# Performance work log

Measured on AMD Instinct MI355X. Metric: run time of the kernel, lower is better.

Reference implementation:

```python
import jax, jax.numpy as jnp
import numpy as np

B, C, H, W = 8, 256, 96, 96
CQ = C // 8

def conv1x1(x, w, b):
    # x: (B,C,H,W), w: (O,C), b: (O,)
    return jnp.einsum('bchw,oc->bohw', x, w) + b[None, :, None, None]

def axial_attend(q, k, v):
    # q,k: (B,CQ,H,W); v: (B,C,H,W). Criss-cross attention with masked diagonal
    # on the column (H) branch and joint softmax over H+W logits.
    Hn = q.shape[2]
    e_h = jnp.einsum('bchw,bcgw->bhwg', q, k)            # (B,H,W,H), g = h'
    eye = jnp.eye(Hn, dtype=bool)
    e_h = jnp.where(eye[None, :, None, :], -jnp.inf, e_h)  # mask h'==h (self on column)
    e_w = jnp.einsum('bchw,bchv->bhwv', q, k)            # (B,H,W,W), v = w'
    attn = jax.nn.softmax(jnp.concatenate([e_h, e_w], axis=-1), axis=-1)
    a_h, a_w = attn[..., :Hn], attn[..., Hn:]
    out_h = jnp.einsum('bcgw,bhwg->bchw', v, a_h)
    out_w = jnp.einsum('bchv,bhwv->bchw', v, a_w)
    return out_h + out_w

def setup_inputs() -> dict:
    key = jax.random.key(0)
    ks = jax.random.split(key, 16)
    s = lambda k, shape, scale=1.0: (jax.random.normal(k, shape, dtype=jnp.float32) * scale)
    return {
        'x0': s(ks[0], (B, C, H, W)),
        'x1': s(ks[1], (B, C, H, W)),
        'wq0': s(ks[2], (CQ, C), 0.06), 'bq0': s(ks[3], (CQ,), 0.06),
        'wk0': s(ks[4], (CQ, C), 0.06), 'bk0': s(ks[5], (CQ,), 0.06),
        'wv0': s(ks[6], (C, C), 0.06),  'bv0': s(ks[7], (C,), 0.06),
        'wq1': s(ks[8], (CQ, C), 0.06), 'bq1': s(ks[9], (CQ,), 0.06),
        'wk1': s(ks[10], (CQ, C), 0.06), 'bk1': s(ks[11], (CQ,), 0.06),
        'wv1': s(ks[12], (C, C), 0.06),  'bv1': s(ks[13], (C,), 0.06),
        'gamma': s(ks[14], (1,)),
    }

def reference(x0, x1, wq0, bq0, wk0, bk0, wv0, bv0, wq1, bq1, wk1, bk1, wv1, bv1, gamma):
    q0 = conv1x1(x0, wq0, bq0); k0 = conv1x1(x0, wk0, bk0); v0 = conv1x1(x0, wv0, bv0)
    q1 = conv1x1(x1, wq1, bq1); k1 = conv1x1(x1, wk1, bk1); v1 = conv1x1(x1, wv1, bv1)
    g = gamma[0]
    # stream 0 output: queries from stream 1, keys/values from stream 0
    cat0 = g * axial_attend(q1, k0, v0) + x0
    # stream 1 output: queries from stream 0, keys/values from stream 1
    cat1 = g * axial_attend(q0, k1, v1) + x1
    return (cat0, cat1)
```

## Files before the change

kernel.cpp:

```cpp
#include <hip/hip_runtime.h>
#include <hip/hip_bf16.h>


#define Bn 8
#define Cn 256
#define NHW 9216
#define PT_BS ((size_t)NHW * 64)

typedef unsigned short u16;
typedef __attribute__((ext_vector_type(8))) _Float16 f16x8;
typedef __attribute__((ext_vector_type(4))) float f32x4;

__device__ __forceinline__ float h2f(u16 v) {
  _Float16 h;
  __builtin_memcpy(&h, &v, 2);
  return (float)h;
}
__device__ __forceinline__ u16 f2h(float f) {
  _Float16 h = (_Float16)f;
  u16 v;
  __builtin_memcpy(&v, &h, 2);
  return v;
}

__global__ __launch_bounds__(256) void pack_all(const float* __restrict__ wq0, const float* __restrict__ bq0,
                                                const float* __restrict__ wk0, const float* __restrict__ bk0,
                                                const float* __restrict__ wv0, const float* __restrict__ bv0,
                                                const float* __restrict__ wq1, const float* __restrict__ bq1,
                                                const float* __restrict__ wk1, const float* __restrict__ bk1,
                                                const float* __restrict__ wv1, const float* __restrict__ bv1,
                                                u16* __restrict__ Wall0, float* __restrict__ ball0,
                                                u16* __restrict__ Wall1, float* __restrict__ ball1) {
  const int pr = blockIdx.y;
  const float* wq = pr ? wq1 : wq0;
  const float* bq = pr ? bq1 : bq0;
  const float* wk = pr ? wk1 : wk0;
  const float* bk = pr ? bk1 : bk0;
  const float* wv = pr ? wv1 : wv0;
  const float* bv = pr ? bv1 : bv0;
  u16* Wall = pr ? Wall1 : Wall0;
  float* ball = pr ? ball1 : ball0;
  int i = blockIdx.x * 256 + threadIdx.x;
  if (i < 320 * 256) {
    int o = i >> 8, c = i & 255;
    float v = (o < 32) ? wq[o * 256 + c] : (o < 64) ? wk[(o - 32) * 256 + c] : wv[(o - 64) * 256 + c];
    Wall[i] = f2h(v);
  }
  if (i < 320) ball[i] = (i < 32) ? bq[i] : (i < 64) ? bk[i - 32] : bv[i - 64];
}

__global__ __launch_bounds__(512, 4) void proj_all(const float* __restrict__ X0, const float* __restrict__ X1,
                                                   const u16* __restrict__ Wall0, const u16* __restrict__ Wall1,
                                                   const float* __restrict__ ball0, const float* __restrict__ ball1,
                                                   u16* __restrict__ Pt0, u16* __restrict__ Pt1,
                                                   u16* __restrict__ vW0, u16* __restrict__ vW1) {
  __shared__ __align__(16) u16 xs[96 * 264];
  u16* sO = xs;
  const int h = blockIdx.x, b = blockIdx.y, pr = blockIdx.z;
  const float* X = pr ? X1 : X0;
  const u16* Wall = pr ? Wall1 : Wall0;
  const float* ball = pr ? ball1 : ball0;
  u16* Pt = pr ? Pt1 : Pt0;
  u16* vW = pr ? vW1 : vW0;
  const int tid = threadIdx.x;
  const float* Xb = X + (size_t)b * Cn * NHW + h * 96;
  const int tcq = tid / 24, tn4 = tid % 24;
  const bool act = tid < 384;
  const int lane = tid & 63, wv = tid >> 6;
  const int mg = wv >> 1, ng = wv & 1;
  const int arow = lane & 15;
  const int g = lane >> 4;
  const int kc = g * 8;
  const u16* wrow[5];
#pragma unroll
  for (int j = 0; j < 5; ++j)
    wrow[j] = Wall + (size_t)((mg + 4 * j) * 16 + arow) * 256 + kc;
  int rbase[3], rsw[3];
#pragma unroll
  for (int nt = 0; nt < 3; ++nt) {
    int row = ng * 48 + nt * 16 + arow;
    rbase[nt] = row * 264;
    rsw[nt] = ((row >> 2) & 7) << 3;
  }
  float4 pre[4];
  if (act) {
    const float* src = Xb + (size_t)(4 * tcq) * NHW + tn4 * 4;
#pragma unroll
    for (int j = 0; j < 4; ++j) pre[j] = *(const float4*)(src + (size_t)j * NHW);
    int colb = (4 * tcq) ^ ((tn4 & 7) << 3);
#pragma unroll
    for (int i = 0; i < 4; ++i) {
      ushort4 wv4;
      wv4.x = f2h(((const float*)&pre[0])[i]);
      wv4.y = f2h(((const float*)&pre[1])[i]);
      wv4.z = f2h(((const float*)&pre[2])[i]);
      wv4.w = f2h(((const float*)&pre[3])[i]);
      *(ushort4*)&xs[(4 * tn4 + i) * 264 + colb] = wv4;
    }
  }
  __syncthreads();
  f32x4 acc[5][3] = {};
#pragma unroll
  for (int q = 0; q < 4; ++q) {
    if (q < 3 && act) {
      const float* src = Xb + (size_t)((q + 1) * 64 + 4 * tcq) * NHW + tn4 * 4;
#pragma unroll
      for (int j = 0; j < 4; ++j) pre[j] = *(const float4*)(src + (size_t)j * NHW);
    }
#pragma unroll
    for (int kk = 2 * q; kk < 2 * q + 2; ++kk) {
      f16x8 a5[5], b3[3];
#pragma unroll
      for (int j = 0; j < 5; ++j) a5[j] = *(const f16x8*)(wrow[j] + kk * 32);
#pragma unroll
      for (int nt = 0; nt < 3; ++nt)
        b3[nt] = *(const f16x8*)&xs[rbase[nt] + ((kk * 32 + kc) ^ rsw[nt])];
#pragma unroll
      for (int j = 0; j < 5; ++j)
#pragma unroll
        for (int nt = 0; nt < 3; ++nt)
          acc[j][nt] = __builtin_amdgcn_mfma_f32_16x16x32_f16(a5[j], b3[nt], acc[j][nt], 0, 0, 0);
    }
    if (q < 3) {
      if (act) {
        int colb = ((q + 1) * 64 + 4 * tcq) ^ ((tn4 & 7) << 3);
#pragma unroll
        for (int i = 0; i < 4; ++i) {
          ushort4 wv4;
          wv4.x = f2h(((const float*)&pre[0])[i]);
          wv4.y = f2h(((const float*)&pre[1])[i]);
          wv4.z = f2h(((const float*)&pre[2])[i]);
          wv4.w = f2h(((const float*)&pre[3])[i]);
          *(ushort4*)&xs[(4 * tn4 + i) * 264 + colb] = wv4;
        }
      }
      __syncthreads();
    }
  }
  {
    u16* Ptb = Pt + (size_t)b * PT_BS;
    float4 bv = *(const float4*)(ball + mg * 16 + (g << 2));
#pragma unroll
    for (int nt = 0; nt < 3; ++nt) {
      int n = h * 96 + ng * 48 + nt * 16 + arow;
      f32x4 a = acc[0][nt];
      ushort4 r;
      r.x = f2h(a[0] + bv.x); r.y = f2h(a[1] + bv.y);
      r.z = f2h(a[2] + bv.z); r.w = f2h(a[3] + bv.w);
      *(ushort4*)&Ptb[(size_t)n * 64 + mg * 16 + (g << 2)] = r;
    }
  }
  __syncthreads();
  for (int r = 0; r < 2; ++r) {
#pragma unroll
    for (int jj = 0; jj < 2; ++jj) {
      int j = 2 * r + 1 + jj;
      int vt = mg + 8 * r + 4 * jj;
      float4 bv = *(const float4*)(ball + 64 + vt * 16 + (g << 2));
      float ba[4] = {bv.x, bv.y, bv.z, bv.w};
      int lrow0 = (mg + 4 * jj) * 16 + (g << 2);
#pragma unroll
      for (int nt = 0; nt < 3; ++nt) {
        int col = ng * 48 + nt * 16 + arow;
#pragma unroll
        for (int rr = 0; rr < 4; ++rr)
          sO[(lrow0 + rr) * 104 + col] = f2h(acc[j][nt][rr] + ba[rr]);
      }
    }
    __syncthreads();
    for (int idx = tid; idx < 1536; idx += 512) {
      int cc = idx / 12, c4 = idx % 12;
      *(float4*)(vW + ((size_t)(b * 96 + h) * 256 + r * 128 + cc) * 96 + c4 * 8) =
          *(const float4*)&sO[cc * 104 + c4 * 8];
    }
    __syncthreads();
  }
}

__global__ __launch_bounds__(256) void vtrans(const u16* __restrict__ vW0, const u16* __restrict__ vW1,
                                              u16* __restrict__ vH0, u16* __restrict__ vH1) {
  __shared__ u16 t[96][98];
  const int c = blockIdx.x, b = blockIdx.y;
  const u16* vWp = blockIdx.z ? vW1 : vW0;
  u16* vHp = blockIdx.z ? vH1 : vH0;
  for (int idx = threadIdx.x; idx < 4608; idx += 256) {
    int hh = idx / 48, w2 = idx % 48;
    *(unsigned int*)&t[hh][w2 * 2] =
        *(const unsigned int*)(vWp + (size_t)(b * 96 + hh) * 24576 + c * 96 + w2 * 2);
  }
  __syncthreads();
  for (int idx = threadIdx.x; idx < 4608; idx += 256) {
    int ww = idx / 48, g2 = idx % 48;
    unsigned int lo = t[g2 * 2][ww];
    unsigned int hi = t[g2 * 2 + 1][ww];
    *(unsigned int*)(vHp + (size_t)(b * 96 + ww) * 24576 + c * 96 + g2 * 2) = lo | (hi << 16);
  }
}

__global__ __launch_bounds__(384, 3) void attn_fused(const u16* __restrict__ Pt0, const u16* __restrict__ Pt1,
                                                     const u16* __restrict__ vW0, const u16* __restrict__ vH0,
                                                     const u16* __restrict__ vW1, const u16* __restrict__ vH1,
                                                     float* __restrict__ mWs, float* __restrict__ sWs,
                                                     float* __restrict__ mHs, float* __restrict__ sHs,
                                                     u16* __restrict__ tmpW0, u16* __restrict__ tmpH0,
                                                     u16* __restrict__ tmpW1, u16* __restrict__ tmpH1) {
  __shared__ __align__(16) char smem[46592];
  u16* vbuf = (u16*)smem;
  u16* qs = (u16*)smem;
  u16* ks = (u16*)(smem + 7680);
  u16* probs = (u16*)(smem + 26624);
  const int p = blockIdx.x, b = blockIdx.y, z = blockIdx.z;
  const int pass = z & 1, pair = z >> 1;
  const u16* Qpt = pair ? Pt0 : Pt1;
  const u16* Kpt = pair ? Pt1 : Pt0;
  const u16* Vp = pair ? (pass ? vH1 : vW1) : (pass ? vH0 : vW0);
  u16* tOut = pair ? (pass ? tmpH1 : tmpW1) : (pass ? tmpH0 : tmpW0);
  float* mOut = (pass ? mHs : mWs) + (size_t)pair * (Bn * 9216);
  float* sOut = (pass ? sHs : sWs) + (size_t)pair * (Bn * 9216);
  const int tid = threadIdx.x;
  const size_t nbase = (size_t)b * PT_BS;
  const size_t rowoff = pass ? (size_t)p * 64 : (size_t)p * 6144;
  const int rstride = pass ? 6144 : 64;
  for (int idx = tid; idx < 768; idx += 384) {
    int i = idx >> 3, c8 = idx & 7;
    const u16* src = (c8 < 4)
        ? Qpt + nbase + rowoff + (size_t)i * rstride + c8 * 8
        : Kpt + nbase + rowoff + (size_t)i * rstride + 32 + (c8 - 4) * 8;
    float4 v = *(const float4*)src;
    u16* dst = (c8 < 4) ? &qs[i * 40 + c8 * 8] : &ks[i * 40 + (c8 - 4) * 8];
    *(float4*)dst = v;
  }
  __syncthreads();
  const int lane = tid & 63, wv = tid >> 6;
  const int cl = lane & 15, g = lane >> 4;
  const int kc = g * 8;
  const int w0 = wv * 16;
  f32x4 eacc[6];
  {
    f16x8 aq = *(const f16x8*)&qs[(w0 + cl) * 40 + kc];
#pragma unroll
    for (int nt = 0; nt < 6; ++nt) {
      f16x8 bk = *(const f16x8*)&ks[(nt * 16 + cl) * 40 + kc];
      f32x4 zz = {0.f, 0.f, 0.f, 0.f};
      eacc[nt] = __builtin_amdgcn_mfma_f32_16x16x32_f16(aq, bk, zz, 0, 0, 0);
    }
  }
#pragma unroll
  for (int r = 0; r < 4; ++r) {
    int i = w0 + 4 * g + r;
    float m = -1e30f;
#pragma unroll
    for (int nt = 0; nt < 6; ++nt) {
      float e = eacc[nt][r];
      if (pass && (nt * 16 + cl) == i) { e = -1e30f; eacc[nt][r] = e; }
      m = fmaxf(m, e);
    }
    m = fmaxf(m, __shfl_xor(m, 1));
    m = fmaxf(m, __shfl_xor(m, 2));
    m = fmaxf(m, __shfl_xor(m, 4));
    m = fmaxf(m, __shfl_xor(m, 8));
    float s = 0.f;
#pragma unroll
    for (int nt = 0; nt < 6; ++nt) {
      float pv = __expf(eacc[nt][r] - m);
      eacc[nt][r] = pv;
      s += pv;
    }
    s += __shfl_xor(s, 1);
    s += __shfl_xor(s, 2);
    s += __shfl_xor(s, 4);
    s += __shfl_xor(s, 8);
#pragma unroll
    for (int nt = 0; nt < 6; ++nt)
      probs[i * 104 + nt * 16 + cl] = f2h(eacc[nt][r]);
    if (cl == 0) {
      size_t sidx = pass ? ((size_t)(b * 96 + i) * 96 + p) : ((size_t)(b * 96 + p) * 96 + i);
      mOut[sidx] = m;
      sOut[sidx] = s;
    }
  }
  __syncthreads();
  f16x8 af[3];
#pragma unroll
  for (int kt = 0; kt < 3; ++kt)
    af[kt] = *(const f16x8*)&probs[(w0 + cl) * 104 + kt * 32 + kc];
  const size_t vbase = (size_t)(b * 96 + p) * 24576;
  for (int half = 0; half < 2; ++half) {
    for (int idx = tid; idx < 1536; idx += 384) {
      int r = idx / 12, c4 = idx % 12;
      *(float4*)&vbuf[r * 104 + c4 * 8] =
          *(const float4*)(Vp + vbase + (size_t)(half * 128 + r) * 96 + c4 * 8);
    }
    __syncthreads();
    f32x4 acc[8];
#pragma unroll
    for (int nt = 0; nt < 8; ++nt) {
      f32x4 a = {0.f, 0.f, 0.f, 0.f};
#pragma unroll
      for (int kt = 0; kt < 3; ++kt) {
        f16x8 bf = *(const f16x8*)&vbuf[(nt * 16 + cl) * 104 + kt * 32 + kc];
        a = __builtin_amdgcn_mfma_f32_16x16x32_f16(af[kt], bf, a, 0, 0, 0);
      }
      acc[nt] = a;
    }
    __syncthreads();
#pragma unroll
    for (int nt = 0; nt < 8; ++nt) {
      int c2 = nt * 16 + cl;
      int wr = w0 + (g << 2);
#pragma unroll
      for (int r = 0; r < 4; ++r) vbuf[c2 * 104 + wr + r] = f2h(acc[nt][r]);
    }
    __syncthreads();
    for (int idx = tid; idx < 1536; idx += 384) {
      int r = idx / 12, c4 = idx % 12;
      *(float4*)(tOut + vbase + (size_t)(half * 128 + r) * 96 + c4 * 8) =
          *(const float4*)&vbuf[r * 104 + c4 * 8];
    }
    __syncthreads();
  }
}

__global__ __launch_bounds__(256) void scl_k(const float* __restrict__ mH, const float* __restrict__ sH,
                                             const float* __restrict__ mW, const float* __restrict__ sW,
                                             const float* __restrict__ gammaP, float* __restrict__ sclH,
                                             float* __restrict__ sclW) {
  int i = blockIdx.x * 256 + threadIdx.x;
  if (i >= 2 * Bn * 9216) return;
  float mh = mH[i], mw = mW[i];
  float m = fmaxf(mh, mw);
  float eh = __expf(mh - m), ew = __expf(mw - m);
  float s = sH[i] * eh + sW[i] * ew;
  float g = gammaP[0] / s;
  sclH[i] = g * eh;
  sclW[i] = g * ew;
}

__global__ __launch_bounds__(256) void tkomb(const u16* __restrict__ tmpH0, const u16* __restrict__ tmpW0,
                                             const u16* __restrict__ tmpH1, const u16* __restrict__ tmpW1,
                                             const float* __restrict__ x0, const float* __restrict__ x1,
                                             const float* __restrict__ sclH, const float* __restrict__ sclW,
                                             float* __restrict__ out) {
  __shared__ u16 t[96][108];
  const int c = blockIdx.x, b = blockIdx.y, pr = blockIdx.z;
  const u16* tmpH = pr ? tmpH1 : tmpH0;
  const u16* tmpW = pr ? tmpW1 : tmpW0;
  const float* x = pr ? x1 : x0;
  const float* sH = sclH + (size_t)pr * (Bn * 9216);
  const float* sW = sclW + (size_t)pr * (Bn * 9216);
  float* o = out + (size_t)pr * Bn * Cn * NHW;
  const int tid = threadIdx.x;
  for (int idx = tid; idx < 2304; idx += 256) {
    int w_ = idx / 24, h4 = idx % 24;
    *(ushort4*)&t[w_][h4 * 4] =
        *(const ushort4*)(tmpH + ((size_t)(b * 96 + w_) * 256 + c) * 96 + h4 * 4);
  }
  __syncthreads();
  for (int idx = tid; idx < 2304; idx += 256) {
    int h_ = idx / 24, w4 = idx % 24;
    size_t go = ((size_t)(b * 256 + c) * 96 + h_) * 96 + w4 * 4;
    float4 xv = *(const float4*)(x + go);
    ushort4 wvv = *(const ushort4*)(tmpW + ((size_t)(b * 96 + h_) * 256 + c) * 96 + w4 * 4);
    float4 sh4 = *(const float4*)(sH + (size_t)(b * 96 + h_) * 96 + w4 * 4);
    float4 sw4 = *(const float4*)(sW + (size_t)(b * 96 + h_) * 96 + w4 * 4);
    float4 ov;
    ov.x = xv.x + h2f(t[w4 * 4 + 0][h_]) * sh4.x + h2f(wvv.x) * sw4.x;
    ov.y = xv.y + h2f(t[w4 * 4 + 1][h_]) * sh4.y + h2f(wvv.y) * sw4.y;
    ov.z = xv.z + h2f(t[w4 * 4 + 2][h_]) * sh4.z + h2f(wvv.z) * sw4.z;
    ov.w = xv.w + h2f(t[w4 * 4 + 3][h_]) * sh4.w + h2f(wvv.w) * sw4.w;
    *(float4*)(o + go) = ov;
  }
}

extern "C" void kernel_launch(void* const* d_in, const int* in_sizes, int n_in,
                              void* d_out, int out_size, void* d_ws, size_t ws_size,
                              hipStream_t stream) {
  const float* x0 = (const float*)d_in[0];
  const float* x1 = (const float*)d_in[1];
  const float* wq0 = (const float*)d_in[2];
  const float* bq0 = (const float*)d_in[3];
  const float* wk0 = (const float*)d_in[4];
  const float* bk0 = (const float*)d_in[5];
  const float* wv0 = (const float*)d_in[6];
  const float* bv0 = (const float*)d_in[7];
  const float* wq1 = (const float*)d_in[8];
  const float* bq1 = (const float*)d_in[9];
  const float* wk1 = (const float*)d_in[10];
  const float* bk1 = (const float*)d_in[11];
  const float* wv1 = (const float*)d_in[12];
  const float* bv1 = (const float*)d_in[13];
  const float* gamma = (const float*)d_in[14];
  float* out = (float*)d_out;

  char* ws = (char*)d_ws;
  size_t off = 0;
  auto alloc = [&](size_t bytes) -> void* {
    void* ptr = ws + off;
    off += (bytes + 255) & ~(size_t)255;
    return ptr;
  };
  const size_t SZ_P = (size_t)Bn * NHW * 64 * 2;
  const size_t SZ_V = (size_t)Bn * NHW * Cn * 2;
  const size_t SZ_S = (size_t)Bn * 9216 * 4;
  u16* Pt0 = (u16*)alloc(SZ_P);
  u16* Pt1 = (u16*)alloc(SZ_P);
  u16* vW0 = (u16*)alloc(SZ_V);
  u16* vW1 = (u16*)alloc(SZ_V);
  u16* vH0 = (u16*)alloc(SZ_V);
  u16* vH1 = (u16*)alloc(SZ_V);
  u16* tmpW0 = (u16*)alloc(SZ_V);
  u16* tmpH0 = (u16*)alloc(SZ_V);
  u16* tmpW1 = (u16*)alloc(SZ_V);
  u16* tmpH1 = (u16*)alloc(SZ_V);
  u16* Wall0 = (u16*)alloc(320 * 256 * 2);
  u16* Wall1 = (u16*)alloc(320 * 256 * 2);
  float* ball0 = (float*)alloc(320 * 4);
  float* ball1 = (float*)alloc(320 * 4);
  float* mH = (float*)alloc(2 * SZ_S);
  float* sH = (float*)alloc(2 * SZ_S);
  float* mW = (float*)alloc(2 * SZ_S);
  float* sW = (float*)alloc(2 * SZ_S);
  float* sclH = (float*)alloc(2 * SZ_S);
  float* sclW = (float*)alloc(2 * SZ_S);
  (void)ws_size; (void)in_sizes; (void)n_in; (void)out_size;

  dim3 gpk(320, 2), gp(96, Bn, 2), gt(256, Bn, 2), ga(96, Bn, 4), gc(256, Bn, 2);
  pack_all<<<gpk, 256, 0, stream>>>(wq0, bq0, wk0, bk0, wv0, bv0,
                                    wq1, bq1, wk1, bk1, wv1, bv1,
                                    Wall0, ball0, Wall1, ball1);
  proj_all<<<gp, 512, 0, stream>>>(x0, x1, Wall0, Wall1, ball0, ball1, Pt0, Pt1, vW0, vW1);
  vtrans<<<gt, 256, 0, stream>>>(vW0, vW1, vH0, vH1);
  attn_fused<<<ga, 384, 0, stream>>>(Pt0, Pt1, vW0, vH0, vW1, vH1,
                                     mW, sW, mH, sH, tmpW0, tmpH0, tmpW1, tmpH1);
  scl_k<<<576, 256, 0, stream>>>(mH, sH, mW, sW, gamma, sclH, sclW);
  tkomb<<<gc, 256, 0, stream>>>(tmpH0, tmpW0, tmpH1, tmpW1, x0, x1, sclH, sclW, out);
}
```

Measured before the change: 320.3 us.

## Fuse row-pass attention with softmax merge and residual combine kernel

Splits the fused attention into a column pass, which writes its unnormalized output transposed to channel-last, and a row pass that also merges the two softmax statistics, scales the probabilities, and writes the final gamma-weighted residual output directly. This removes the scl_k and tkomb kernels, the tmpW buffers and the mW/sW/scl arrays, which cuts a large amount of fp16 intermediate traffic and two launches. The two passes now run serially as separate kernels instead of concurrently in one grid, and the combine step reads tH with a transposed LDS tile that has a strided access pattern.

```diff
diff --git a/kernel.cpp b/kernel.cpp
--- a/kernel.cpp
+++ b/kernel.cpp
@@ -197,30 +197,26 @@
   }
 }
 
-__global__ __launch_bounds__(384, 3) void attn_fused(const u16* __restrict__ Pt0, const u16* __restrict__ Pt1,
-                                                     const u16* __restrict__ vW0, const u16* __restrict__ vH0,
-                                                     const u16* __restrict__ vW1, const u16* __restrict__ vH1,
-                                                     float* __restrict__ mWs, float* __restrict__ sWs,
-                                                     float* __restrict__ mHs, float* __restrict__ sHs,
-                                                     u16* __restrict__ tmpW0, u16* __restrict__ tmpH0,
-                                                     u16* __restrict__ tmpW1, u16* __restrict__ tmpH1) {
+__global__ __launch_bounds__(384, 3) void attn1(const u16* __restrict__ Pt0, const u16* __restrict__ Pt1,
+                                                const u16* __restrict__ vH0, const u16* __restrict__ vH1,
+                                                float* __restrict__ mHs, float* __restrict__ sHs,
+                                                u16* __restrict__ tHt0, u16* __restrict__ tHt1) {
   __shared__ __align__(16) char smem[46592];
   u16* vbuf = (u16*)smem;
   u16* qs = (u16*)smem;
   u16* ks = (u16*)(smem + 7680);
   u16* probs = (u16*)(smem + 26624);
-  const int p = blockIdx.x, b = blockIdx.y, z = blockIdx.z;
-  const int pass = z & 1, pair = z >> 1;
+  const int p = blockIdx.x, b = blockIdx.y, pair = blockIdx.z;
   const u16* Qpt = pair ? Pt0 : Pt1;
   const u16* Kpt = pair ? Pt1 : Pt0;
-  const u16* Vp = pair ? (pass ? vH1 : vW1) : (pass ? vH0 : vW0);
-  u16* tOut = pair ? (pass ? tmpH1 : tmpW1) : (pass ? tmpH0 : tmpW0);
-  float* mOut = (pass ? mHs : mWs) + (size_t)pair * (Bn * 9216);
-  float* sOut = (pass ? sHs : sWs) + (size_t)pair * (Bn * 9216);
+  const u16* Vp = pair ? vH1 : vH0;
+  u16* tOut = pair ? tHt1 : tHt0;
+  float* mOut = mHs + (size_t)pair * (Bn * 9216);
+  float* sOut = sHs + (size_t)pair * (Bn * 9216);
   const int tid = threadIdx.x;
   const size_t nbase = (size_t)b * PT_BS;
-  const size_t rowoff = pass ? (size_t)p * 64 : (size_t)p * 6144;
-  const int rstride = pass ? 6144 : 64;
+  const size_t rowoff = (size_t)p * 64;
+  const int rstride = 6144;
   for (int idx = tid; idx < 768; idx += 384) {
     int i = idx >> 3, c8 = idx & 7;
     const u16* src = (c8 < 4)
@@ -252,7 +248,7 @@
 #pragma unroll
     for (int nt = 0; nt < 6; ++nt) {
       float e = eacc[nt][r];
-      if (pass && (nt * 16 + cl) == i) { e = -1e30f; eacc[nt][r] = e; }
+      if ((nt * 16 + cl) == i) { e = -1e30f; eacc[nt][r] = e; }
       m = fmaxf(m, e);
     }
     m = fmaxf(m, __shfl_xor(m, 1));
@@ -274,7 +270,7 @@
     for (int nt = 0; nt < 6; ++nt)
       probs[i * 104 + nt * 16 + cl] = f2h(eacc[nt][r]);
     if (cl == 0) {
-      size_t sidx = pass ? ((size_t)(b * 96 + i) * 96 + p) : ((size_t)(b * 96 + p) * 96 + i);
+      size_t sidx = (size_t)(b * 96 + i) * 96 + p;
       mOut[sidx] = m;
       sOut[sidx] = s;
     }
@@ -309,66 +305,171 @@
       int c2 = nt * 16 + cl;
       int wr = w0 + (g << 2);
 #pragma unroll
-      for (int r = 0; r < 4; ++r) vbuf[c2 * 104 + wr + r] = f2h(acc[nt][r]);
-    }
-    __syncthreads();
+      for (int r = 0; r < 4; ++r) vbuf[(wr + r) * 136 + c2] = f2h(acc[nt][r]);
+    }
+    __syncthreads();
+    for (int idx = tid; idx < 1536; idx += 384) {
+      int i = idx >> 4, c8 = idx & 15;
+      *(float4*)(tOut + ((size_t)(b * 96 + p) * 96 + i) * 256 + half * 128 + c8 * 8) =
+          *(const float4*)&vbuf[i * 136 + c8 * 8];
+    }
+    __syncthreads();
+  }
+}
+
+__global__ __launch_bounds__(384, 3) void pv_comb(const u16* __restrict__ Pt0, const u16* __restrict__ Pt1,
+                                                  const u16* __restrict__ vW0, const u16* __restrict__ vW1,
+                                                  const float* __restrict__ mHs, const float* __restrict__ sHs,
+                                                  const u16* __restrict__ tHt0, const u16* __restrict__ tHt1,
+                                                  const float* __restrict__ x0, const float* __restrict__ x1,
+                                                  const float* __restrict__ gammaP, float* __restrict__ out) {
+  __shared__ __align__(16) char smem[50432];
+  u16* vbuf = (u16*)smem;
+  u16* qs = (u16*)smem;
+  u16* ks = (u16*)(smem + 7680);
+  u16* probs = (u16*)(smem + 26624);
+  u16* ttile = (u16*)smem;
+  float* sclh = (float*)(smem + 49920);
+  const int p = blockIdx.x, b = blockIdx.y, pair = blockIdx.z;
+  const u16* Qpt = pair ? Pt0 : Pt1;
+  const u16* Kpt = pair ? Pt1 : Pt0;
+  const u16* Vp = pair ? vW1 : vW0;
+  const u16* tH = pair ? tHt1 : tHt0;
+  const float* x = pair ? x1 : x0;
+  const float* mH = mHs + (size_t)pair * (Bn * 9216);
+  const float* sH = sHs + (size_t)pair * (Bn * 9216);
+  float* o = out + (size_t)pair * Bn * Cn * NHW;
+  const int tid = threadIdx.x;
+  const size_t nbase = (size_t)b * PT_BS;
+  const size_t rowoff = (size_t)p * 6144;
+  for (int idx = tid; idx < 768; idx += 384) {
+    int i = idx >> 3, c8 = idx & 7;
+    const u16* src = (c8 < 4)
+        ? Qpt + nbase + rowoff + (size_t)i * 64 + c8 * 8
+        : Kpt + nbase + rowoff + (size_t)i * 64 + 32 + (c8 - 4) * 8;
+    float4 v = *(const float4*)src;
+    u16* dst = (c8 < 4) ? &qs[i * 40 + c8 * 8] : &ks[i * 40 + (c8 - 4) * 8];
+    *(float4*)dst = v;
+  }
+  __syncthreads();
+  const int lane = tid & 63, wv = tid >> 6;
+  const int cl = lane & 15, g = lane >> 4;
+  const int kc = g * 8;
+  const int w0 = wv * 16;
+  f32x4 eacc[6];
+  {
+    f16x8 aq = *(const f16x8*)&qs[(w0 + cl) * 40 + kc];
+#pragma unroll
+    for (int nt = 0; nt < 6; ++nt) {
+      f16x8 bk = *(const f16x8*)&ks[(nt * 16 + cl) * 40 + kc];
+      f32x4 zz = {0.f, 0.f, 0.f, 0.f};
+      eacc[nt] = __builtin_amdgcn_mfma_f32_16x16x32_f16(aq, bk, zz, 0, 0, 0);
+    }
+  }
+  const float gam = gammaP[0];
+#pragma unroll
+  for (int r = 0; r < 4; ++r) {
+    int i = w0 + 4 * g + r;
+    float mw = -1e30f;
+#pragma unroll
+    for (int nt = 0; nt < 6; ++nt) mw = fmaxf(mw, eacc[nt][r]);
+    mw = fmaxf(mw, __shfl_xor(mw, 1));
+    mw = fmaxf(mw, __shfl_xor(mw, 2));
+    mw = fmaxf(mw, __shfl_xor(mw, 4));
+    mw = fmaxf(mw, __shfl_xor(mw, 8));
+    float sw = 0.f;
+#pragma unroll
+    for (int nt = 0; nt < 6; ++nt) {
+      float pv = __expf(eacc[nt][r] - mw);
+      eacc[nt][r] = pv;
+      sw += pv;
+    }
+    sw += __shfl_xor(sw, 1);
+    sw += __shfl_xor(sw, 2);
+    sw += __shfl_xor(sw, 4);
+    sw += __shfl_xor(sw, 8);
+    size_t sidx = (size_t)(b * 96 + p) * 96 + i;
+    float mh = mH[sidx], sh = sH[sidx];
+    float m = fmaxf(mh, mw);
+    float eh_ = __expf(mh - m), ew_ = __expf(mw - m);
+    float s = sh * eh_ + sw * ew_;
+    float gm = gam / s;
+    float sclW = gm * ew_;
+#pragma unroll
+    for (int nt = 0; nt < 6; ++nt)
+      probs[i * 104 + nt * 16 + cl] = f2h(eacc[nt][r] * sclW);
+    if (cl == 0) sclh[i] = gm * eh_;
+  }
+  __syncthreads();
+  f16x8 af[3];
+#pragma unroll
+  for (int kt = 0; kt < 3; ++kt)
+    af[kt] = *(const f16x8*)&probs[(w0 + cl) * 104 + kt * 32 + kc];
+  const size_t vbase = (size_t)(b * 96 + p) * 24576;
+  float4 ro[2][4];
+  for (int half = 0; half < 2; ++half) {
     for (int idx = tid; idx < 1536; idx += 384) {
       int r = idx / 12, c4 = idx % 12;
-      *(float4*)(tOut + vbase + (size_t)(half * 128 + r) * 96 + c4 * 8) =
-          *(const float4*)&vbuf[r * 104 + c4 * 8];
-    }
-    __syncthreads();
-  }
-}
-
-__global__ __launch_bounds__(256) void scl_k(const float* __restrict__ mH, const float* __restrict__ sH,
-                                             const float* __restrict__ mW, const float* __restrict__ sW,
-                                             const float* __restrict__ gammaP, float* __restrict__ sclH,
-                                             float* __restrict__ sclW) {
-  int i = blockIdx.x * 256 + threadIdx.x;
-  if (i >= 2 * Bn * 9216) return;
-  float mh = mH[i], mw = mW[i];
-  float m = fmaxf(mh, mw);
-  float eh = __expf(mh - m), ew = __expf(mw - m);
-  float s = sH[i] * eh + sW[i] * ew;
-  float g = gammaP[0] / s;
-  sclH[i] = g * eh;
-  sclW[i] = g * ew;
-}
-
-__global__ __launch_bounds__(256) void tkomb(const u16* __restrict__ tmpH0, const u16* __restrict__ tmpW0,
-                                             const u16* __restrict__ tmpH1, const u16* __restrict__ tmpW1,
-                                             const float* __restrict__ x0, const float* __restrict__ x1,
-                                             const float* __restrict__ sclH, const float* __restrict__ sclW,
-                                             float* __restrict__ out) {
-  __shared__ u16 t[96][108];
-  const int c = blockIdx.x, b = blockIdx.y, pr = blockIdx.z;
-  const u16* tmpH = pr ? tmpH1 : tmpH0;
-  const u16* tmpW = pr ? tmpW1 : tmpW0;
-  const float* x = pr ? x1 : x0;
-  const float* sH = sclH + (size_t)pr * (Bn * 9216);
-  const float* sW = sclW + (size_t)pr * (Bn * 9216);
-  float* o = out + (size_t)pr * Bn * Cn * NHW;
-  const int tid = threadIdx.x;
-  for (int idx = tid; idx < 2304; idx += 256) {
-    int w_ = idx / 24, h4 = idx % 24;
-    *(ushort4*)&t[w_][h4 * 4] =
-        *(const ushort4*)(tmpH + ((size_t)(b * 96 + w_) * 256 + c) * 96 + h4 * 4);
-  }
-  __syncthreads();
-  for (int idx = tid; idx < 2304; idx += 256) {
-    int h_ = idx / 24, w4 = idx % 24;
-    size_t go = ((size_t)(b * 256 + c) * 96 + h_) * 96 + w4 * 4;
-    float4 xv = *(const float4*)(x + go);
-    ushort4 wvv = *(const ushort4*)(tmpW + ((size_t)(b * 96 + h_) * 256 + c) * 96 + w4 * 4);
-    float4 sh4 = *(const float4*)(sH + (size_t)(b * 96 + h_) * 96 + w4 * 4);
-    float4 sw4 = *(const float4*)(sW + (size_t)(b * 96 + h_) * 96 + w4 * 4);
-    float4 ov;
-    ov.x = xv.x + h2f(t[w4 * 4 + 0][h_]) * sh4.x + h2f(wvv.x) * sw4.x;
-    ov.y = xv.y + h2f(t[w4 * 4 + 1][h_]) * sh4.y + h2f(wvv.y) * sw4.y;
-    ov.z = xv.z + h2f(t[w4 * 4 + 2][h_]) * sh4.z + h2f(wvv.z) * sw4.z;
-    ov.w = xv.w + h2f(t[w4 * 4 + 3][h_]) * sh4.w + h2f(wvv.w) * sw4.w;
-    *(float4*)(o + go) = ov;
+      *(float4*)&vbuf[r * 104 + c4 * 8] =
+          *(const float4*)(Vp + vbase + (size_t)(half * 128 + r) * 96 + c4 * 8);
+    }
+    __syncthreads();
+    f32x4 acc[8];
+#pragma unroll
+    for (int nt = 0; nt < 8; ++nt) {
+      f32x4 a = {0.f, 0.f, 0.f, 0.f};
+#pragma unroll
+      for (int kt = 0; kt < 3; ++kt) {
+        f16x8 bf = *(const f16x8*)&vbuf[(nt * 16 + cl) * 104 + kt * 32 + kc];
+        a = __builtin_amdgcn_mfma_f32_16x16x32_f16(af[kt], bf, a, 0, 0, 0);
+      }
+      acc[nt] = a;
+    }
+    __syncthreads();
+#pragma unroll
+    for (int nt = 0; nt < 8; ++nt) {
+      int c2 = nt * 16 + cl;
+      int wr = w0 + (g << 2);
+#pragma unroll
+      for (int r = 0; r < 4; ++r) vbuf[c2 * 104 + wr + r] = f2h(acc[nt][r]);
+    }
+    __syncthreads();
+#pragma unroll
+    for (int k = 0; k < 4; ++k) {
+      int idx = tid + k * 384;
+      int cc = idx / 12, c4 = idx % 12;
+      ro[half][k] = *(const float4*)&vbuf[cc * 104 + c4 * 8];
+    }
+    __syncthreads();
+  }
+  for (int idx = tid; idx < 3072; idx += 384) {
+    int w = idx >> 5, c16 = idx & 31;
+    *(float4*)&ttile[w * 260 + c16 * 8] =
+        *(const float4*)(tH + ((size_t)(b * 96 + w) * 96 + p) * 256 + c16 * 8);
+  }
+  __syncthreads();
+#pragma unroll
+  for (int half = 0; half < 2; ++half) {
+#pragma unroll
+    for (int k = 0; k < 4; ++k) {
+      int idx = tid + k * 384;
+      int cc = idx / 12, c4 = idx % 12;
+      int C = half * 128 + cc;
+      size_t go = ((size_t)(b * 256 + C) * 96 + p) * 96 + c4 * 8;
+      float4 xv0 = *(const float4*)(x + go);
+      float4 xv1 = *(const float4*)(x + go + 4);
+      const u16* rw = (const u16*)&ro[half][k];
+      float r0[8];
+#pragma unroll
+      for (int j = 0; j < 8; ++j) {
+        int wj = c4 * 8 + j;
+        r0[j] = h2f(rw[j]) + h2f(ttile[wj * 260 + C]) * sclh[wj];
+      }
+      float4 ov0 = make_float4(xv0.x + r0[0], xv0.y + r0[1], xv0.z + r0[2], xv0.w + r0[3]);
+      float4 ov1 = make_float4(xv1.x + r0[4], xv1.y + r0[5], xv1.z + r0[6], xv1.w + r0[7]);
+      *(float4*)(o + go) = ov0;
+      *(float4*)(o + go + 4) = ov1;
+    }
   }
 }
 
@@ -408,30 +509,22 @@
   u16* vW1 = (u16*)alloc(SZ_V);
   u16* vH0 = (u16*)alloc(SZ_V);
   u16* vH1 = (u16*)alloc(SZ_V);
-  u16* tmpW0 = (u16*)alloc(SZ_V);
-  u16* tmpH0 = (u16*)alloc(SZ_V);
-  u16* tmpW1 = (u16*)alloc(SZ_V);
-  u16* tmpH1 = (u16*)alloc(SZ_V);
+  u16* tHt0 = (u16*)alloc(SZ_V);
+  u16* tHt1 = (u16*)alloc(SZ_V);
   u16* Wall0 = (u16*)alloc(320 * 256 * 2);
   u16* Wall1 = (u16*)alloc(320 * 256 * 2);
   float* ball0 = (float*)alloc(320 * 4);
   float* ball1 = (float*)alloc(320 * 4);
   float* mH = (float*)alloc(2 * SZ_S);
   float* sH = (float*)alloc(2 * SZ_S);
-  float* mW = (float*)alloc(2 * SZ_S);
-  float* sW = (float*)alloc(2 * SZ_S);
-  float* sclH = (float*)alloc(2 * SZ_S);
-  float* sclW = (float*)alloc(2 * SZ_S);
   (void)ws_size; (void)in_sizes; (void)n_in; (void)out_size;
 
-  dim3 gpk(320, 2), gp(96, Bn, 2), gt(256, Bn, 2), ga(96, Bn, 4), gc(256, Bn, 2);
+  dim3 gpk(320, 2), gp(96, Bn, 2), gt(256, Bn, 2), ga(96, Bn, 2);
   pack_all<<<gpk, 256, 0, stream>>>(wq0, bq0, wk0, bk0, wv0, bv0,
                                     wq1, bq1, wk1, bk1, wv1, bv1,
                                     Wall0, ball0, Wall1, ball1);
   proj_all<<<gp, 512, 0, stream>>>(x0, x1, Wall0, Wall1, ball0, ball1, Pt0, Pt1, vW0, vW1);
   vtrans<<<gt, 256, 0, stream>>>(vW0, vW1, vH0, vH1);
-  attn_fused<<<ga, 384, 0, stream>>>(Pt0, Pt1, vW0, vH0, vW1, vH1,
-                                     mW, sW, mH, sH, tmpW0, tmpH0, tmpW1, tmpH1);
-  scl_k<<<576, 256, 0, stream>>>(mH, sH, mW, sW, gamma, sclH, sclW);
-  tkomb<<<gc, 256, 0, stream>>>(tmpH0, tmpW0, tmpH1, tmpW1, x0, x1, sclH, sclW, out);
-}
+  attn1<<<ga, 384, 0, stream>>>(Pt0, Pt1, vH0, vH1, mH, sH, tHt0, tHt1);
+  pv_comb<<<ga, 384, 0, stream>>>(Pt0, Pt1, vW0, vW1, mH, sH, tHt0, tHt1, x0, x1, gamma, out);
+}
```

New measurement: 292.3 us, median of 2. 1.1x faster.
